# Optimization experiments

Measured on AMD Instinct MI355X. Metric: run time of the kernel, lower is better.

The kernel has to match this reference:

```python
import jax, jax.numpy as jnp
import numpy as np

B, H, T, N, DK = 4, 8, 12, 325, 32


def setup_inputs() -> dict:
    key = jax.random.key(0)
    ks = jax.random.split(key, 8)
    shp = (B, H, T, N, DK)
    return {
        "Qf": jax.random.normal(ks[0], shp, jnp.float32),
        "Kf": jax.random.normal(ks[1], shp, jnp.float32),
        "Vf": jax.random.normal(ks[2], shp, jnp.float32),
        "Qs": jax.random.normal(ks[3], shp, jnp.float32),
        "Ks": jax.random.normal(ks[4], shp, jnp.float32),
        "Vs": jax.random.normal(ks[5], shp, jnp.float32),
        "Kj": jax.random.normal(ks[6], (N, 1), jnp.float32),   # FlowSpeed jam density param
        "Vf_p": jax.random.normal(ks[7], (N, 1), jnp.float32),  # FlowSpeed free-flow speed param
    }


def reference(Qf, Kf, Vf, Qs, Ks, Vs, Kj, Vf_p):
    d_k = Qf.shape[-1]
    scale = 1.0 / np.sqrt(d_k).astype(np.float32)

    # FlowSpeed nonlinearity: flow = Kj * (speed - speed^2 / (Vf + 1e-5))
    # Kj, Vf_p: (N,1) broadcast over (..., N, d_k)
    Qf_from_speed = Kj * (Qs - jnp.square(Qs) / (Vf_p + 1e-5))

    def attn(q, k, v):
        # q,k,v: [B,H,T,N,dk]; scores: [B,H,T,N,N]
        scores = jnp.einsum("bhtnd,bhtmd->bhtnm", q, k) * scale
        return jnp.einsum("bhtnm,bhtmd->bhtnd", jax.nn.softmax(scores, axis=-1), v)

    context_flow_flow = attn(Qf, Kf, Vf)
    context_flow_speed = attn(Kf, Qf_from_speed, Vf)
    context_speed_flow = attn(Ks, Qf, Vs)
    context_speed_speed = attn(Qs, Ks, Vs)
    return (context_flow_flow, context_flow_speed, context_speed_flow, context_speed_speed)
```

## Files before the change

### kernel.cpp

```cpp
#include <hip/hip_runtime.h>
#include <hip/hip_bf16.h>

typedef float f32x4 __attribute__((ext_vector_type(4)));
typedef short short8 __attribute__((ext_vector_type(8)));

#define NT    325
#define DKK   32
#define NSL   384
#define SLICE (NT*DKK)
#define TOTE  (NSL*SLICE)
#define NKT   21
#define PADV  352
#define VGRAN (32 * (PADV/8))
#define SCALE2 0.25506372f

__device__ __forceinline__ int swz(int sidx, int row) { return sidx ^ ((row & 7) << 3); }

__device__ __forceinline__ unsigned cvtpk(float lo, float hi) {
    unsigned r;
    asm("v_cvt_pk_bf16_f32 %0, %1, %2" : "=v"(r) : "v"(lo), "v"(hi));
    return r;
}
__device__ __forceinline__ unsigned pk2_split(float x, float y, unsigned& lopk) {
    const unsigned hi = cvtpk(x, y);
    const float hx = __builtin_bit_cast(float, hi << 16);
    const float hy = __builtin_bit_cast(float, hi & 0xffff0000u);
    lopk = cvtpk(x - hx, y - hy);
    return hi;
}
__device__ __forceinline__ void swap32(unsigned& a, unsigned& b) {
    asm("v_permlane32_swap_b32 %0, %1" : "+v"(a), "+v"(b));
}
__device__ __forceinline__ void swap16(unsigned& a, unsigned& b) {
    asm("v_permlane16_swap_b32 %0, %1" : "+v"(a), "+v"(b));
}
__device__ __forceinline__ short8 repack(const f32x4& a0, const f32x4& a1, bool hasB) {
    unsigned u = cvtpk(a0[0], a0[1]);
    unsigned v = cvtpk(a0[2], a0[3]);
    unsigned s = hasB ? cvtpk(a1[0], a1[1]) : 0u;
    unsigned t = hasB ? cvtpk(a1[2], a1[3]) : 0u;
    swap32(u, s); swap16(u, s);
    swap32(v, t); swap16(v, t);
    uint4 w; w.x = u; w.y = v; w.z = s; w.w = t;
    return __builtin_bit_cast(short8, w);
}

__global__ __launch_bounds__(512, 2)
void attn4_mfma(const float* __restrict__ Qf, const float* __restrict__ Kf,
                const float* __restrict__ Vf, const float* __restrict__ Qs,
                const float* __restrict__ Ks, const float* __restrict__ Vs,
                const float* __restrict__ Kj, const float* __restrict__ Vfp,
                float* __restrict__ out)
{
    __shared__ __align__(16) unsigned short Kb[336 * DKK];
    __shared__ __align__(16) unsigned short Kl[336 * DKK];
    __shared__ __align__(16) unsigned short Vt[DKK * PADV];

    const int tid = threadIdx.x;
    const int bid = blockIdx.x;
    const int g8  = bid >> 3, xx = bid & 7;
    const int var = (xx + g8) & 3;
    const int bt  = 2 * g8 + (xx >> 2);
    const size_t base = (size_t)bt * SLICE;

    const float *qp, *kp, *vp;
    if      (var == 0) { qp = Qf; kp = Kf; vp = Vf; }
    else if (var == 1) { qp = Kf; kp = Qs; vp = Vf; }
    else if (var == 2) { qp = Ks; kp = Qf; vp = Vs; }
    else               { qp = Qs; kp = Ks; vp = Vs; }
    float* op = out + (size_t)var * TOTE + base;

    for (int i8 = tid; i8 < SLICE / 8; i8 += 512) {
        const int idx = i8 * 8;
        const int m   = idx >> 5;
        const int sidx = swz(idx, m);
        const float* s = kp + base + idx;
        float4 a = *(const float4*)s;
        float4 b = *(const float4*)(s + 4);
        if (var == 1) {
            const float kj = Kj[m];
            const float rv = 1.0f / (Vfp[m] + 1e-5f);
            a.x = kj * (a.x - a.x * a.x * rv);
            a.y = kj * (a.y - a.y * a.y * rv);
            a.z = kj * (a.z - a.z * a.z * rv);
            a.w = kj * (a.w - a.w * a.w * rv);
            b.x = kj * (b.x - b.x * b.x * rv);
            b.y = kj * (b.y - b.y * b.y * rv);
            b.z = kj * (b.z - b.z * b.z * rv);
            b.w = kj * (b.w - b.w * b.w * rv);
            uint4 hw, lw;
            hw.x = pk2_split(a.x, a.y, lw.x);
            hw.y = pk2_split(a.z, a.w, lw.y);
            hw.z = pk2_split(b.x, b.y, lw.z);
            hw.w = pk2_split(b.z, b.w, lw.w);
            *(uint4*)&Kb[sidx] = hw;
            *(uint4*)&Kl[sidx] = lw;
        } else {
            uint4 pkv;
            pkv.x = cvtpk(a.x, a.y); pkv.y = cvtpk(a.z, a.w);
            pkv.z = cvtpk(b.x, b.y); pkv.w = cvtpk(b.z, b.w);
            *(uint4*)&Kb[sidx] = pkv;
        }
    }

    for (int gi = tid; gi < VGRAN; gi += 512) {
        const int dd = gi / 44;
        const int m8 = gi - dd * 44;
        const int mb = m8 * 8;
        float v[8];
        #pragma unroll
        for (int i = 0; i < 8; ++i) {
            const int m = mb + i;
            v[i] = (m < NT) ? vp[base + (size_t)m * DKK + dd] : 0.0f;
        }
        uint4 pkv;
        pkv.x = cvtpk(v[0], v[1]); pkv.y = cvtpk(v[2], v[3]);
        pkv.z = cvtpk(v[4], v[5]); pkv.w = cvtpk(v[6], v[7]);
        *(uint4*)&Vt[swz(dd * PADV + mb, dd)] = pkv;
    }
    __syncthreads();

    const int lane = tid & 63;
    const int wv   = tid >> 6;
    const int c    = lane & 15;
    const int g    = lane >> 4;
    const int kswz = (c & 7) << 3;
    const f32x4 zero = {0.f, 0.f, 0.f, 0.f};

    int qt = wv;
    float4 qa, qb;
    {
        int qr = qt * 16 + c; if (qr > NT - 1) qr = NT - 1;
        const float* s = qp + base + (size_t)qr * DKK + g * 8;
        qa = *(const float4*)s; qb = *(const float4*)(s + 4);
    }

    for (; qt < NKT; qt += 8) {
        float4 na, nb;
        const bool more = (qt + 8) < NKT;
        if (more) {
            int qr = (qt + 8) * 16 + c; if (qr > NT - 1) qr = NT - 1;
            const float* s = qp + base + (size_t)qr * DKK + g * 8;
            na = *(const float4*)s; nb = *(const float4*)(s + 4);
        }

        uint4 qwh, qwl;
        qwh.x = pk2_split(qa.x * SCALE2, qa.y * SCALE2, qwl.x);
        qwh.y = pk2_split(qa.z * SCALE2, qa.w * SCALE2, qwl.y);
        qwh.z = pk2_split(qb.x * SCALE2, qb.y * SCALE2, qwl.z);
        qwh.w = pk2_split(qb.z * SCALE2, qb.w * SCALE2, qwl.w);
        const short8 qh = __builtin_bit_cast(short8, qwh);
        const short8 ql = __builtin_bit_cast(short8, qwl);

        f32x4 o0 = zero, o1 = zero;
        float ts = 0.f;
        float mrow = -1e30f;

        #pragma unroll
        for (int ks = 0; ks < 11; ++ks) {
            const int fi0 = (((2 * ks) * 16 + c) * DKK + g * 8) ^ kswz;
            const int fi1 = fi0 + 16 * DKK;
            const bool hasB1 = (ks < 10);
            f32x4 a0, a1;

            __builtin_amdgcn_s_setprio(1);
            if (var != 1) {
                const short8 k0 = *(const short8*)&Kb[fi0];
                a0 = __builtin_amdgcn_mfma_f32_16x16x32_bf16(k0, qh, zero, 0, 0, 0);
                if (hasB1) {
                    const short8 k1 = *(const short8*)&Kb[fi1];
                    a1 = __builtin_amdgcn_mfma_f32_16x16x32_bf16(k1, qh, zero, 0, 0, 0);
                }
            } else {
                {
                    const short8 kh = *(const short8*)&Kb[fi0];
                    const short8 kl = *(const short8*)&Kl[fi0];
                    f32x4 t = __builtin_amdgcn_mfma_f32_16x16x32_bf16(kh, ql, zero, 0, 0, 0);
                    t = __builtin_amdgcn_mfma_f32_16x16x32_bf16(kl, qh, t, 0, 0, 0);
                    a0 = __builtin_amdgcn_mfma_f32_16x16x32_bf16(kh, qh, t, 0, 0, 0);
                }
                if (hasB1) {
                    const short8 kh = *(const short8*)&Kb[fi1];
                    const short8 kl = *(const short8*)&Kl[fi1];
                    f32x4 t = __builtin_amdgcn_mfma_f32_16x16x32_bf16(kh, ql, zero, 0, 0, 0);
                    t = __builtin_amdgcn_mfma_f32_16x16x32_bf16(kl, qh, t, 0, 0, 0);
                    a1 = __builtin_amdgcn_mfma_f32_16x16x32_bf16(kh, qh, t, 0, 0, 0);
                }
            }
            __builtin_amdgcn_s_setprio(0);

            if (ks == 10) {
                #pragma unroll
                for (int r = 0; r < 4; ++r)
                    a0[r] = (4 * g + r > 4) ? -1e30f : a0[r];
            }

            if (var == 1) {
                float pm = fmaxf(fmaxf(a0[0], a0[1]), fmaxf(a0[2], a0[3]));
                if (hasB1)
                    pm = fmaxf(pm, fmaxf(fmaxf(a1[0], a1[1]), fmaxf(a1[2], a1[3])));
                pm = fmaxf(pm, __shfl_xor(pm, 16));
                pm = fmaxf(pm, __shfl_xor(pm, 32));
                if (__any(pm > mrow)) {
                    const float mn = fmaxf(mrow, pm);
                    const float f = exp2f(mrow - mn);
                    mrow = mn; ts *= f;
                    #pragma unroll
                    for (int r = 0; r < 4; ++r) {
                        const float fr = __shfl(f, 4 * g + r);
                        o0[r] *= fr; o1[r] *= fr;
                    }
                }
                #pragma unroll
                for (int r = 0; r < 4; ++r) { a0[r] = exp2f(a0[r] - mrow); ts += a0[r]; }
                if (hasB1) {
                    #pragma unroll
                    for (int r = 0; r < 4; ++r) { a1[r] = exp2f(a1[r] - mrow); ts += a1[r]; }
                }
            } else {
                #pragma unroll
                for (int r = 0; r < 4; ++r) { a0[r] = exp2f(a0[r]); ts += a0[r]; }
                if (hasB1) {
                    #pragma unroll
                    for (int r = 0; r < 4; ++r) { a1[r] = exp2f(a1[r]); ts += a1[r]; }
                }
            }

            const short8 af = repack(a0, hasB1 ? a1 : a0, hasB1);
            const short8 v0 = *(const short8*)&Vt[( c        * PADV + ks * 32 + g * 8) ^ kswz];
            const short8 v1 = *(const short8*)&Vt[((c + 16)  * PADV + ks * 32 + g * 8) ^ kswz];
            __builtin_amdgcn_s_setprio(1);
            o0 = __builtin_amdgcn_mfma_f32_16x16x32_bf16(af, v0, o0, 0, 0, 0);
            o1 = __builtin_amdgcn_mfma_f32_16x16x32_bf16(af, v1, o1, 0, 0, 0);
            __builtin_amdgcn_s_setprio(0);
        }

        ts += __shfl_xor(ts, 16);
        ts += __shfl_xor(ts, 32);
        const float inv = 1.0f / ts;

        #pragma unroll
        for (int r = 0; r < 4; ++r) {
            const int row = qt * 16 + 4 * g + r;
            const float iv = __shfl(inv, 4 * g + r);
            if (row < NT) {
                op[(size_t)row * DKK + c]      = o0[r] * iv;
                op[(size_t)row * DKK + c + 16] = o1[r] * iv;
            }
        }
        qa = na; qb = nb;
    }
}

extern "C" void kernel_launch(void* const* d_in, const int* in_sizes, int n_in,
                              void* d_out, int out_size, void* d_ws, size_t ws_size,
                              hipStream_t stream) {
    const float* Qf  = (const float*)d_in[0];
    const float* Kf  = (const float*)d_in[1];
    const float* Vf  = (const float*)d_in[2];
    const float* Qs  = (const float*)d_in[3];
    const float* Ks  = (const float*)d_in[4];
    const float* Vs  = (const float*)d_in[5];
    const float* Kj  = (const float*)d_in[6];
    const float* Vfp = (const float*)d_in[7];
    float* out = (float*)d_out;

    attn4_mfma<<<dim3(NSL * 4), dim3(512), 0, stream>>>(Qf, Kf, Vf, Qs, Ks, Vs, Kj, Vfp, out);
}
```

Before: 115.7 us.

## Split attention into slim bf16 kernel and fat split-precision kernel

Splits the single kernel that handled all four attention variants into two launches. One kernel covers the three plain variants using only the bf16 K buffer, with no online-max logic and launch bounds raised to 3 blocks per CU. The other covers the FlowSpeed variant with hi/lo split-precision and online softmax. The aim is to stop the slim variants paying the fat variant's LDS and register footprint, so occupancy can rise, at the cost of a second launch and a serialized tail from the smaller fat grid.

```diff
diff --git a/kernel.cpp b/kernel.cpp
--- a/kernel.cpp
+++ b/kernel.cpp
@@ -45,30 +45,167 @@
     return __builtin_bit_cast(short8, w);
 }
 
+__global__ __launch_bounds__(512, 3)
+void attn_slim(const float* __restrict__ Qf, const float* __restrict__ Kf,
+               const float* __restrict__ Vf, const float* __restrict__ Qs,
+               const float* __restrict__ Ks, const float* __restrict__ Vs,
+               float* __restrict__ out)
+{
+    __shared__ __align__(16) unsigned short Kb[336 * DKK];
+    __shared__ __align__(16) unsigned short Vt[DKK * PADV];
+
+    const int tid = threadIdx.x;
+    const int bid = blockIdx.x;
+    const int bt  = bid / 3;
+    const int vr  = bid - 3 * bt;
+    const int vi  = (vr + bt) % 3;
+    const int var = (vi == 0) ? 0 : (vi == 1) ? 2 : 3;
+    const size_t base = (size_t)bt * SLICE;
+
+    const float *qp, *kp, *vp;
+    if      (var == 0) { qp = Qf; kp = Kf; vp = Vf; }
+    else if (var == 2) { qp = Ks; kp = Qf; vp = Vs; }
+    else               { qp = Qs; kp = Ks; vp = Vs; }
+    float* op = out + (size_t)var * TOTE + base;
+
+    for (int i8 = tid; i8 < SLICE / 8; i8 += 512) {
+        const int idx = i8 * 8;
+        const int m   = idx >> 5;
+        const float* s = kp + base + idx;
+        const float4 a = *(const float4*)s;
+        const float4 b = *(const float4*)(s + 4);
+        uint4 pkv;
+        pkv.x = cvtpk(a.x, a.y); pkv.y = cvtpk(a.z, a.w);
+        pkv.z = cvtpk(b.x, b.y); pkv.w = cvtpk(b.z, b.w);
+        *(uint4*)&Kb[swz(idx, m)] = pkv;
+    }
+
+    for (int gi = tid; gi < VGRAN; gi += 512) {
+        const int dd = gi / 44;
+        const int m8 = gi - dd * 44;
+        const int mb = m8 * 8;
+        float v[8];
+        #pragma unroll
+        for (int i = 0; i < 8; ++i) {
+            const int m = mb + i;
+            v[i] = (m < NT) ? vp[base + (size_t)m * DKK + dd] : 0.0f;
+        }
+        uint4 pkv;
+        pkv.x = cvtpk(v[0], v[1]); pkv.y = cvtpk(v[2], v[3]);
+        pkv.z = cvtpk(v[4], v[5]); pkv.w = cvtpk(v[6], v[7]);
+        *(uint4*)&Vt[swz(dd * PADV + mb, dd)] = pkv;
+    }
+    __syncthreads();
+
+    const int lane = tid & 63;
+    const int wv   = tid >> 6;
+    const int c    = lane & 15;
+    const int g    = lane >> 4;
+    const int kswz = (c & 7) << 3;
+    const f32x4 zero = {0.f, 0.f, 0.f, 0.f};
+
+    int qt = wv;
+    float4 qa, qb;
+    {
+        int qr = qt * 16 + c; if (qr > NT - 1) qr = NT - 1;
+        const float* s = qp + base + (size_t)qr * DKK + g * 8;
+        qa = *(const float4*)s; qb = *(const float4*)(s + 4);
+    }
+
+    for (; qt < NKT; qt += 8) {
+        float4 na, nb;
+        const bool more = (qt + 8) < NKT;
+        if (more) {
+            int qr = (qt + 8) * 16 + c; if (qr > NT - 1) qr = NT - 1;
+            const float* s = qp + base + (size_t)qr * DKK + g * 8;
+            na = *(const float4*)s; nb = *(const float4*)(s + 4);
+        }
+
+        uint4 qwh;
+        qwh.x = cvtpk(qa.x * SCALE2, qa.y * SCALE2);
+        qwh.y = cvtpk(qa.z * SCALE2, qa.w * SCALE2);
+        qwh.z = cvtpk(qb.x * SCALE2, qb.y * SCALE2);
+        qwh.w = cvtpk(qb.z * SCALE2, qb.w * SCALE2);
+        const short8 qh = __builtin_bit_cast(short8, qwh);
+
+        f32x4 o0 = zero, o1 = zero;
+        float ts = 0.f;
+
+        #pragma unroll
+        for (int ks = 0; ks < 11; ++ks) {
+            const int fi0 = (((2 * ks) * 16 + c) * DKK + g * 8) ^ kswz;
+            const int fi1 = fi0 + 16 * DKK;
+            const bool hasB1 = (ks < 10);
+            f32x4 a0, a1;
+
+            __builtin_amdgcn_s_setprio(1);
+            {
+                const short8 k0 = *(const short8*)&Kb[fi0];
+                a0 = __builtin_amdgcn_mfma_f32_16x16x32_bf16(k0, qh, zero, 0, 0, 0);
+                if (hasB1) {
+                    const short8 k1 = *(const short8*)&Kb[fi1];
+                    a1 = __builtin_amdgcn_mfma_f32_16x16x32_bf16(k1, qh, zero, 0, 0, 0);
+                }
+            }
+            __builtin_amdgcn_s_setprio(0);
+
+            if (ks == 10) {
+                #pragma unroll
+                for (int r = 0; r < 4; ++r)
+                    a0[r] = (4 * g + r > 4) ? -1e30f : a0[r];
+            }
+
+            #pragma unroll
+            for (int r = 0; r < 4; ++r) { a0[r] = exp2f(a0[r]); ts += a0[r]; }
+            if (hasB1) {
+                #pragma unroll
+                for (int r = 0; r < 4; ++r) { a1[r] = exp2f(a1[r]); ts += a1[r]; }
+            }
+
+            const short8 af = repack(a0, hasB1 ? a1 : a0, hasB1);
+            const short8 v0 = *(const short8*)&Vt[( c        * PADV + ks * 32 + g * 8) ^ kswz];
+            const short8 v1 = *(const short8*)&Vt[((c + 16)  * PADV + ks * 32 + g * 8) ^ kswz];
+            __builtin_amdgcn_s_setprio(1);
+            o0 = __builtin_amdgcn_mfma_f32_16x16x32_bf16(af, v0, o0, 0, 0, 0);
+            o1 = __builtin_amdgcn_mfma_f32_16x16x32_bf16(af, v1, o1, 0, 0, 0);
+            __builtin_amdgcn_s_setprio(0);
+        }
+
+        ts += __shfl_xor(ts, 16);
+        ts += __shfl_xor(ts, 32);
+        const float inv = 1.0f / ts;
+
+        #pragma unroll
+        for (int r = 0; r < 4; ++r) {
+            const int row = qt * 16 + 4 * g + r;
+            const float iv = __shfl(inv, 4 * g + r);
+            if (row < NT) {
+                op[(size_t)row * DKK + c]      = o0[r] * iv;
+                op[(size_t)row * DKK + c + 16] = o1[r] * iv;
+            }
+        }
+        qa = na; qb = nb;
+    }
+}
+
 __global__ __launch_bounds__(512, 2)
-void attn4_mfma(const float* __restrict__ Qf, const float* __restrict__ Kf,
-                const float* __restrict__ Vf, const float* __restrict__ Qs,
-                const float* __restrict__ Ks, const float* __restrict__ Vs,
-                const float* __restrict__ Kj, const float* __restrict__ Vfp,
-                float* __restrict__ out)
+void attn_fat(const float* __restrict__ Kf, const float* __restrict__ Vf,
+              const float* __restrict__ Qs,
+              const float* __restrict__ Kj, const float* __restrict__ Vfp,
+              float* __restrict__ out)
 {
     __shared__ __align__(16) unsigned short Kb[336 * DKK];
     __shared__ __align__(16) unsigned short Kl[336 * DKK];
     __shared__ __align__(16) unsigned short Vt[DKK * PADV];
 
     const int tid = threadIdx.x;
-    const int bid = blockIdx.x;
-    const int g8  = bid >> 3, xx = bid & 7;
-    const int var = (xx + g8) & 3;
-    const int bt  = 2 * g8 + (xx >> 2);
+    const int bt  = blockIdx.x;
     const size_t base = (size_t)bt * SLICE;
 
-    const float *qp, *kp, *vp;
-    if      (var == 0) { qp = Qf; kp = Kf; vp = Vf; }
-    else if (var == 1) { qp = Kf; kp = Qs; vp = Vf; }
-    else if (var == 2) { qp = Ks; kp = Qf; vp = Vs; }
-    else               { qp = Qs; kp = Ks; vp = Vs; }
-    float* op = out + (size_t)var * TOTE + base;
+    const float* qp = Kf;
+    const float* kp = Qs;
+    const float* vp = Vf;
+    float* op = out + (size_t)1 * TOTE + base;
 
     for (int i8 = tid; i8 < SLICE / 8; i8 += 512) {
         const int idx = i8 * 8;
@@ -77,30 +214,23 @@
         const float* s = kp + base + idx;
         float4 a = *(const float4*)s;
         float4 b = *(const float4*)(s + 4);
-        if (var == 1) {
-            const float kj = Kj[m];
-            const float rv = 1.0f / (Vfp[m] + 1e-5f);
-            a.x = kj * (a.x - a.x * a.x * rv);
-            a.y = kj * (a.y - a.y * a.y * rv);
-            a.z = kj * (a.z - a.z * a.z * rv);
-            a.w = kj * (a.w - a.w * a.w * rv);
-            b.x = kj * (b.x - b.x * b.x * rv);
-            b.y = kj * (b.y - b.y * b.y * rv);
-            b.z = kj * (b.z - b.z * b.z * rv);
-            b.w = kj * (b.w - b.w * b.w * rv);
-            uint4 hw, lw;
-            hw.x = pk2_split(a.x, a.y, lw.x);
-            hw.y = pk2_split(a.z, a.w, lw.y);
-            hw.z = pk2_split(b.x, b.y, lw.z);
-            hw.w = pk2_split(b.z, b.w, lw.w);
-            *(uint4*)&Kb[sidx] = hw;
-            *(uint4*)&Kl[sidx] = lw;
-        } else {
-            uint4 pkv;
-            pkv.x = cvtpk(a.x, a.y); pkv.y = cvtpk(a.z, a.w);
-            pkv.z = cvtpk(b.x, b.y); pkv.w = cvtpk(b.z, b.w);
-            *(uint4*)&Kb[sidx] = pkv;
-        }
+        const float kj = Kj[m];
+        const float rv = 1.0f / (Vfp[m] + 1e-5f);
+        a.x = kj * (a.x - a.x * a.x * rv);
+        a.y = kj * (a.y - a.y * a.y * rv);
+        a.z = kj * (a.z - a.z * a.z * rv);
+        a.w = kj * (a.w - a.w * a.w * rv);
+        b.x = kj * (b.x - b.x * b.x * rv);
+        b.y = kj * (b.y - b.y * b.y * rv);
+        b.z = kj * (b.z - b.z * b.z * rv);
+        b.w = kj * (b.w - b.w * b.w * rv);
+        uint4 hw, lw;
+        hw.x = pk2_split(a.x, a.y, lw.x);
+        hw.y = pk2_split(a.z, a.w, lw.y);
+        hw.z = pk2_split(b.x, b.y, lw.z);
+        hw.w = pk2_split(b.z, b.w, lw.w);
+        *(uint4*)&Kb[sidx] = hw;
+        *(uint4*)&Kl[sidx] = lw;
     }
 
     for (int gi = tid; gi < VGRAN; gi += 512) {
@@ -164,28 +294,19 @@
             f32x4 a0, a1;
 
             __builtin_amdgcn_s_setprio(1);
-            if (var != 1) {
-                const short8 k0 = *(const short8*)&Kb[fi0];
-                a0 = __builtin_amdgcn_mfma_f32_16x16x32_bf16(k0, qh, zero, 0, 0, 0);
-                if (hasB1) {
-                    const short8 k1 = *(const short8*)&Kb[fi1];
-                    a1 = __builtin_amdgcn_mfma_f32_16x16x32_bf16(k1, qh, zero, 0, 0, 0);
-                }
-            } else {
-                {
-                    const short8 kh = *(const short8*)&Kb[fi0];
-                    const short8 kl = *(const short8*)&Kl[fi0];
-                    f32x4 t = __builtin_amdgcn_mfma_f32_16x16x32_bf16(kh, ql, zero, 0, 0, 0);
-                    t = __builtin_amdgcn_mfma_f32_16x16x32_bf16(kl, qh, t, 0, 0, 0);
-                    a0 = __builtin_amdgcn_mfma_f32_16x16x32_bf16(kh, qh, t, 0, 0, 0);
-                }
-                if (hasB1) {
-                    const short8 kh = *(const short8*)&Kb[fi1];
-                    const short8 kl = *(const short8*)&Kl[fi1];
-                    f32x4 t = __builtin_amdgcn_mfma_f32_16x16x32_bf16(kh, ql, zero, 0, 0, 0);
-                    t = __builtin_amdgcn_mfma_f32_16x16x32_bf16(kl, qh, t, 0, 0, 0);
-                    a1 = __builtin_amdgcn_mfma_f32_16x16x32_bf16(kh, qh, t, 0, 0, 0);
-                }
+            {
+                const short8 kh = *(const short8*)&Kb[fi0];
+                const short8 kl = *(const short8*)&Kl[fi0];
+                f32x4 t = __builtin_amdgcn_mfma_f32_16x16x32_bf16(kh, ql, zero, 0, 0, 0);
+                t = __builtin_amdgcn_mfma_f32_16x16x32_bf16(kl, qh, t, 0, 0, 0);
+                a0 = __builtin_amdgcn_mfma_f32_16x16x32_bf16(kh, qh, t, 0, 0, 0);
+            }
+            if (hasB1) {
+                const short8 kh = *(const short8*)&Kb[fi1];
+                const short8 kl = *(const short8*)&Kl[fi1];
+                f32x4 t = __builtin_amdgcn_mfma_f32_16x16x32_bf16(kh, ql, zero, 0, 0, 0);
+                t = __builtin_amdgcn_mfma_f32_16x16x32_bf16(kl, qh, t, 0, 0, 0);
+                a1 = __builtin_amdgcn_mfma_f32_16x16x32_bf16(kh, qh, t, 0, 0, 0);
             }
             __builtin_amdgcn_s_setprio(0);
 
@@ -195,35 +316,26 @@
                     a0[r] = (4 * g + r > 4) ? -1e30f : a0[r];
             }
 
-            if (var == 1) {
-                float pm = fmaxf(fmaxf(a0[0], a0[1]), fmaxf(a0[2], a0[3]));
-                if (hasB1)
-                    pm = fmaxf(pm, fmaxf(fmaxf(a1[0], a1[1]), fmaxf(a1[2], a1[3])));
-                pm = fmaxf(pm, __shfl_xor(pm, 16));
-                pm = fmaxf(pm, __shfl_xor(pm, 32));
-                if (__any(pm > mrow)) {
-                    const float mn = fmaxf(mrow, pm);
-                    const float f = exp2f(mrow - mn);
-                    mrow = mn; ts *= f;
-                    #pragma unroll
-                    for (int r = 0; r < 4; ++r) {
-                        const float fr = __shfl(f, 4 * g + r);
-                        o0[r] *= fr; o1[r] *= fr;
-                    }
+            float pm = fmaxf(fmaxf(a0[0], a0[1]), fmaxf(a0[2], a0[3]));
+            if (hasB1)
+                pm = fmaxf(pm, fmaxf(fmaxf(a1[0], a1[1]), fmaxf(a1[2], a1[3])));
+            pm = fmaxf(pm, __shfl_xor(pm, 16));
+            pm = fmaxf(pm, __shfl_xor(pm, 32));
+            if (__any(pm > mrow)) {
+                const float mn = fmaxf(mrow, pm);
+                const float f = exp2f(mrow - mn);
+                mrow = mn; ts *= f;
+                #pragma unroll
+                for (int r = 0; r < 4; ++r) {
+                    const float fr = __shfl(f, 4 * g + r);
+                    o0[r] *= fr; o1[r] *= fr;
                 }
-                #pragma unroll
-                for (int r = 0; r < 4; ++r) { a0[r] = exp2f(a0[r] - mrow); ts += a0[r]; }
-                if (hasB1) {
-                    #pragma unroll
-                    for (int r = 0; r < 4; ++r) { a1[r] = exp2f(a1[r] - mrow); ts += a1[r]; }
-                }
-            } else {
-                #pragma unroll
-                for (int r = 0; r < 4; ++r) { a0[r] = exp2f(a0[r]); ts += a0[r]; }
-                if (hasB1) {
-                    #pragma unroll
-                    for (int r = 0; r < 4; ++r) { a1[r] = exp2f(a1[r]); ts += a1[r]; }
-                }
+            }
+            #pragma unroll
+            for (int r = 0; r < 4; ++r) { a0[r] = exp2f(a0[r] - mrow); ts += a0[r]; }
+            if (hasB1) {
+                #pragma unroll
+                for (int r = 0; r < 4; ++r) { a1[r] = exp2f(a1[r] - mrow); ts += a1[r]; }
             }
 
             const short8 af = repack(a0, hasB1 ? a1 : a0, hasB1);
@@ -265,5 +377,6 @@
     const float* Vfp = (const float*)d_in[7];
     float* out = (float*)d_out;
 
-    attn4_mfma<<<dim3(NSL * 4), dim3(512), 0, stream>>>(Qf, Kf, Vf, Qs, Ks, Vs, Kj, Vfp, out);
-}
+    attn_slim<<<dim3(NSL * 3), dim3(512), 0, stream>>>(Qf, Kf, Vf, Qs, Ks, Vs, out);
+    attn_fat <<<dim3(NSL),     dim3(512), 0, stream>>>(Kf, Vf, Qs, Kj, Vfp, out);
+}
```

New measurement: 114.5 us. About the same (-1.0%).
